# Performance work log

Hardware: AMD Instinct MI355X
Metric: run time of the kernel (lower is better)

Reference implementation:

```python
import jax, jax.numpy as jnp
import numpy as np

SIZE = 128      # reconstruction grid (size x size)
ANGLES = 128    # number of projection angles after interpolation
B, C, H, W = 2, 8, 128, 128  # batch, channels, detector rows (z-slices), detector cols
N_VIEWS = 8


def setup_inputs() -> dict:
    key = jax.random.key(0)
    keys = jax.random.split(key, N_VIEWS)
    return {f"f{i}": jax.random.normal(keys[i], (B, C, H, W), dtype=jnp.float32)
            for i in range(N_VIEWS)}


def _fbp(projections, size, n_angles):
    # projections: (B, C, H, V, W) -- V stacked views, W detector columns
    b, c, h, v, w = projections.shape
    # Interpolation step: resize V views -> n_angles angles (linear, half-pixel,
    # matching F.interpolate default semantics)
    sino = jax.image.resize(projections, (b, c, h, n_angles, w), method="linear")
    # Ram-Lak ramp filter along the detector-column axis
    ramp = jnp.abs(jnp.fft.fftfreq(w)).astype(jnp.float32)
    filt = jnp.real(jnp.fft.ifft(jnp.fft.fft(sino, axis=-1) * ramp, axis=-1)).astype(sino.dtype)
    # Back-projection (parallel beam, per z-slice H)
    thetas = jnp.arange(n_angles, dtype=jnp.float32) * (jnp.pi / n_angles)
    xs = jnp.arange(size, dtype=jnp.float32) - (size - 1) / 2.0
    X, Y = jnp.meshgrid(xs, xs, indexing="xy")  # (S, S)
    center = (w - 1) / 2.0

    sino_per_angle = jnp.moveaxis(filt, 3, 0)  # (A, B, C, H, W)

    def body(acc, inputs):
        theta, sino_a = inputs                       # sino_a: (B, C, H, W)
        t = X * jnp.cos(theta) + Y * jnp.sin(theta) + center  # (S, S)
        t = jnp.clip(t, 0.0, w - 1.0)
        t0 = jnp.floor(t).astype(jnp.int32)
        t1 = jnp.minimum(t0 + 1, w - 1)
        w1 = (t - t0).astype(sino_a.dtype)
        v0 = sino_a[..., t0]                         # (B, C, H, S, S) gather
        v1 = sino_a[..., t1]
        acc = acc + v0 * (1.0 - w1) + v1 * w1
        return acc, None

    acc0 = jnp.zeros((b, c, h, size, size), dtype=sino.dtype)
    vol, _ = jax.lax.scan(body, acc0, (thetas, sino_per_angle))
    return vol * (jnp.pi / (2.0 * n_angles))


def reference(f0, f1, f2, f3, f4, f5, f6, f7):
    # torch.cat([f.unsqueeze(3) for f in features], dim=3) == stack on new axis 3
    projections = jnp.stack([f0, f1, f2, f3, f4, f5, f6, f7], axis=3)  # (B,C,H,V,W)
    return _fbp(projections, SIZE, ANGLES)
```

## Files before the change

kernel.cpp:

```cpp
#include <hip/hip_runtime.h>
#include <math.h>

#define W 128
#define NANG 128
#define SZ 128
#define NV 8
#define NROWS 2048
#define K_DIM 1024
#define NPIX 16384
#define OUT_SCALE 0.012271846303085130f

typedef _Float16 f16x8 __attribute__((ext_vector_type(8)));
typedef _Float16 f16x4 __attribute__((ext_vector_type(4)));
typedef float    f32x4 __attribute__((ext_vector_type(4)));

#define PF_OFF 36864
#define WV_OFF (36864 + (size_t)NROWS * K_DIM * 2)

struct Ptrs8 { const float* p[8]; };

__device__ __forceinline__ void glds16(const void* g, void* l) {
    __builtin_amdgcn_global_load_lds(
        (const __attribute__((address_space(1))) void*)g,
        (__attribute__((address_space(3))) void*)l, 16, 0, 0);
}

#define FS_A 136
#define PREP_FG_BLOCKS 256

union PrepLds {
    struct {
        _Float16 sA[64 * FS_A];
        _Float16 sB[128 * FS_A];
        float    kl[W];
    } fg;
    struct {
        float  wrow[8 * K_DIM];
        float2 cst[NANG];
    } wv;
};

__global__ __launch_bounds__(256)
void k_prep(Ptrs8 in, _Float16* __restrict__ pf, _Float16* __restrict__ wv) {
    __shared__ PrepLds u;
    const int tid = threadIdx.x;

    if (blockIdx.x < PREP_FG_BLOCKS) {
        const int blk  = blockIdx.x;
        const int lane = tid & 63, wave = tid >> 6;
        const int fr = lane & 15, fg = lane >> 4;

        if (tid < W) {
            const int d = tid;
            const float w0 = 6.283185307179586f / (float)W * (float)d;
            float s = 0.f;
            for (int f = 1; f < 64; ++f)
                s = fmaf((float)f, __cosf(w0 * (float)f), s);
            s = 2.f * s + 64.f * ((d & 1) ? -1.f : 1.f);
            u.fg.kl[d] = s * (1.f / (float)(W * W));
        }
        {
            const int i   = tid >> 5;
            const int pos = (tid & 31) * 4;
#pragma unroll
            for (int v = 0; v < NV; ++v) {
                float4 x = *(const float4*)(in.p[v] + (size_t)(blk * 8 + i) * W + pos);
                f16x4 h = { (_Float16)x.x, (_Float16)x.y, (_Float16)x.z, (_Float16)x.w };
                *(f16x4*)&u.fg.sA[(i * 8 + v) * FS_A + pos] = h;
            }
        }
        __syncthreads();
        for (int e = tid; e < W * W; e += 256) {
            const int t = e >> 7, s = e & 127;
            u.fg.sB[t * FS_A + s] = (_Float16)u.fg.kl[(t - s) & (W - 1)];
        }
        __syncthreads();

        f32x4 acc[8] = {};
#pragma unroll
        for (int kb = 0; kb < W; kb += 32) {
            f16x8 af = *(const f16x8*)&u.fg.sA[(wave * 16 + fr) * FS_A + kb + fg * 8];
#pragma unroll
            for (int nt = 0; nt < 8; ++nt) {
                f16x8 bf = *(const f16x8*)&u.fg.sB[(nt * 16 + fr) * FS_A + kb + fg * 8];
                acc[nt] = __builtin_amdgcn_mfma_f32_16x16x32_f16(af, bf, acc[nt], 0, 0, 0);
            }
        }
#pragma unroll
        for (int nt = 0; nt < 8; ++nt) {
            int m = blk * 64 + wave * 16 + fg * 4;
            int n = nt * 16 + fr;
#pragma unroll
            for (int rr = 0; rr < 4; ++rr)
                pf[(size_t)(m + rr) * W + n] = (_Float16)acc[nt][rr];
        }
    } else {
        const int p0 = (blockIdx.x - PREP_FG_BLOCKS) * 8;
        if (tid < NANG) {
            float th = (float)tid * ((float)M_PI / (float)NANG);
            u.wv.cst[tid] = make_float2(cosf(th), sinf(th));
        }
        for (int i = tid; i < 8 * K_DIM; i += 256) u.wv.wrow[i] = 0.f;
        __syncthreads();
        const int px  = tid >> 5;
        const int sub = tid & 31;
        const int p = p0 + px;
        const float x = (float)(p & 127) - 63.5f;
        const float y = (float)(p >> 7) - 63.5f;
        float* prow = &u.wv.wrow[px * K_DIM];
        for (int a = sub; a < NANG; a += 32) {
            float2 c = u.wv.cst[a];
            float t = fmaf(x, c.x, fmaf(y, c.y, 63.5f));
            t = fminf(fmaxf(t, 0.f), 127.f);
            float tf = fminf(floorf(t), 126.f);
            int   ti = (int)tf;
            float wt = t - tf;
            float src = ((float)a + 0.5f) * 0.0625f - 0.5f;
            src = fminf(fmaxf(src, 0.f), 7.f);
            float vf = floorf(src);
            int   v0 = (int)vf;
            int   v1 = v0 + 1 < NV ? v0 + 1 : NV - 1;
            float wa = src - vf;
            float wA0 = (1.f - wa) * OUT_SCALE;
            atomicAdd(&prow[v0 * W + ti],     wA0 * (1.f - wt));
            atomicAdd(&prow[v0 * W + ti + 1], wA0 * wt);
            if (v1 != v0) {
                float wA1 = wa * OUT_SCALE;
                atomicAdd(&prow[v1 * W + ti],     wA1 * (1.f - wt));
                atomicAdd(&prow[v1 * W + ti + 1], wA1 * wt);
            }
        }
        __syncthreads();
        uint* wvu = (uint*)(wv + (size_t)p0 * K_DIM);
#pragma unroll
        for (int j = 0; j < 16; ++j) {
            int j2 = tid + 256 * j;
            float2 w2 = *(const float2*)&u.wv.wrow[j2 * 2];
            union { uint uu; struct { _Float16 lo, hi; } h; } pk;
            pk.h.lo = (_Float16)w2.x; pk.h.hi = (_Float16)w2.y;
            wvu[j2] = pk.uu;
        }
    }
}

#define NT 16

__device__ __forceinline__ void fencebar() {
    asm volatile("" ::: "memory");
    __builtin_amdgcn_s_barrier();
    asm volatile("" ::: "memory");
}

__device__ __forceinline__ void stage_half(const _Float16* __restrict__ G, int R0,
                                           int h, int kt, _Float16* L, int tid) {
#pragma unroll
    for (int r = 0; r < 2; ++r) {
        const int c   = r * 512 + tid;
        const int row = (h << 7) + (c >> 3);
        const int q   = c & 7;
        const _Float16* src = G + (size_t)(R0 + row) * K_DIM + kt * 64
                                + ((q ^ (row & 7)) << 3);
        _Float16* dst = L + (h << 13) + ((r * 512 + (tid & 448)) << 3);
        glds16(src, dst);
    }
}

__device__ __forceinline__ f16x8 frag(const _Float16* L, int row, int q) {
    return *(const f16x8*)(L + row * 64 + ((q ^ (row & 7)) << 3));
}

__global__ __launch_bounds__(512, 2)
void k_gemm(const _Float16* __restrict__ A,
            const _Float16* __restrict__ Bm,
            float* __restrict__ out) {
    __shared__ _Float16 lds[65536];
    const int tid  = threadIdx.x;
    const int lane = tid & 63, wid = tid >> 6;
    const int wm = wid >> 2, wn = wid & 3;
    const int fr = lane & 15, fg = lane >> 4;

    const int flat = blockIdx.y * 64 + blockIdx.x;
    const int x    = flat & 7;
    const int idx  = flat >> 3;
    const int m0 = (idx >> 3) * 256;
    const int n0 = (x * 8 + (idx & 7)) * 256;

    _Float16* const A0 = lds;
    _Float16* const B0 = lds + 16384;
    _Float16* const A1 = lds + 32768;
    _Float16* const B1 = lds + 49152;

    stage_half(Bm, n0, 0, 0, B0, tid);
    stage_half(A,  m0, 0, 0, A0, tid);
    stage_half(Bm, n0, 1, 0, B0, tid);
    stage_half(A,  m0, 1, 0, A0, tid);
    stage_half(Bm, n0, 0, 1, B1, tid);
    stage_half(A,  m0, 0, 1, A1, tid);
    asm volatile("s_waitcnt vmcnt(4)" ::: "memory");
    fencebar();

    f32x4 acc[8][4] = {};
    f16x8 af[4][2], bf[4][2];
    const int ar = wm * 128 + fr;
    const int br = wn * 64 + fr;

    auto tile = [&](int t, _Float16* Ab, _Float16* Bb, _Float16* An, _Float16* Bn)
        __attribute__((always_inline)) {
#pragma unroll
        for (int i = 0; i < 4; ++i) {
            af[i][0] = frag(Ab, ar + i * 16, fg);
            af[i][1] = frag(Ab, ar + i * 16, 4 + fg);
        }
#pragma unroll
        for (int j = 0; j < 2; ++j) {
            bf[j][0] = frag(Bb, br + j * 16, fg);
            bf[j][1] = frag(Bb, br + j * 16, 4 + fg);
        }
        if (t + 1 < NT) stage_half(Bm, n0, 1, t + 1, Bn, tid);
        fencebar();
        asm volatile("s_waitcnt lgkmcnt(0)" ::: "memory");
        __builtin_amdgcn_sched_barrier(0);
        __builtin_amdgcn_s_setprio(1);
#pragma unroll
        for (int i = 0; i < 4; ++i)
#pragma unroll
            for (int j = 0; j < 2; ++j) {
                acc[i][j] = __builtin_amdgcn_mfma_f32_16x16x32_f16(af[i][0], bf[j][0], acc[i][j], 0, 0, 0);
                acc[i][j] = __builtin_amdgcn_mfma_f32_16x16x32_f16(af[i][1], bf[j][1], acc[i][j], 0, 0, 0);
            }
        __builtin_amdgcn_s_setprio(0);
        fencebar();
#pragma unroll
        for (int j = 2; j < 4; ++j) {
            bf[j][0] = frag(Bb, br + j * 16, fg);
            bf[j][1] = frag(Bb, br + j * 16, 4 + fg);
        }
        if (t + 1 < NT) stage_half(A, m0, 1, t + 1, An, tid);
        fencebar();
        asm volatile("s_waitcnt lgkmcnt(0)" ::: "memory");
        __builtin_amdgcn_sched_barrier(0);
        __builtin_amdgcn_s_setprio(1);
#pragma unroll
        for (int i = 0; i < 4; ++i)
#pragma unroll
            for (int j = 2; j < 4; ++j) {
                acc[i][j] = __builtin_amdgcn_mfma_f32_16x16x32_f16(af[i][0], bf[j][0], acc[i][j], 0, 0, 0);
                acc[i][j] = __builtin_amdgcn_mfma_f32_16x16x32_f16(af[i][1], bf[j][1], acc[i][j], 0, 0, 0);
            }
        __builtin_amdgcn_s_setprio(0);
        fencebar();
#pragma unroll
        for (int i = 0; i < 4; ++i) {
            af[i][0] = frag(Ab, ar + 64 + i * 16, fg);
            af[i][1] = frag(Ab, ar + 64 + i * 16, 4 + fg);
        }
        if (t + 2 < NT) stage_half(Bm, n0, 0, t + 2, Bb, tid);
        fencebar();
        asm volatile("s_waitcnt lgkmcnt(0)" ::: "memory");
        __builtin_amdgcn_sched_barrier(0);
        __builtin_amdgcn_s_setprio(1);
#pragma unroll
        for (int i = 0; i < 4; ++i)
#pragma unroll
            for (int j = 2; j < 4; ++j) {
                acc[4 + i][j] = __builtin_amdgcn_mfma_f32_16x16x32_f16(af[i][0], bf[j][0], acc[4 + i][j], 0, 0, 0);
                acc[4 + i][j] = __builtin_amdgcn_mfma_f32_16x16x32_f16(af[i][1], bf[j][1], acc[4 + i][j], 0, 0, 0);
            }
        __builtin_amdgcn_s_setprio(0);
        fencebar();
        if (t + 2 < NT) stage_half(A, m0, 0, t + 2, Ab, tid);
        fencebar();
        __builtin_amdgcn_s_setprio(1);
#pragma unroll
        for (int i = 0; i < 4; ++i)
#pragma unroll
            for (int j = 0; j < 2; ++j) {
                acc[4 + i][j] = __builtin_amdgcn_mfma_f32_16x16x32_f16(af[i][0], bf[j][0], acc[4 + i][j], 0, 0, 0);
                acc[4 + i][j] = __builtin_amdgcn_mfma_f32_16x16x32_f16(af[i][1], bf[j][1], acc[4 + i][j], 0, 0, 0);
            }
        __builtin_amdgcn_s_setprio(0);
        if (t + 2 < NT)      asm volatile("s_waitcnt vmcnt(4)" ::: "memory");
        else if (t + 1 < NT) asm volatile("s_waitcnt vmcnt(0)" ::: "memory");
        fencebar();
    };

    for (int tt = 0; tt < NT; tt += 2) {
        tile(tt,     A0, B0, A1, B1);
        tile(tt + 1, A1, B1, A0, B0);
    }

#pragma unroll
    for (int i = 0; i < 8; ++i) {
#pragma unroll
        for (int j = 0; j < 4; ++j) {
            const int m = m0 + wm * 128 + i * 16 + fg * 4;
            const int n = n0 + wn * 64 + j * 16 + fr;
            float* op = out + (size_t)m * NPIX + n;
#pragma unroll
            for (int rr = 0; rr < 4; ++rr)
                op[(size_t)rr * NPIX] = acc[i][j][rr];
        }
    }
}

extern "C" void kernel_launch(void* const* d_in, const int* in_sizes, int n_in,
                              void* d_out, int out_size, void* d_ws, size_t ws_size,
                              hipStream_t stream) {
    _Float16*   pf = (_Float16*)((char*)d_ws + PF_OFF);
    _Float16*   wv = (_Float16*)((char*)d_ws + WV_OFF);

    Ptrs8 in;
    for (int i = 0; i < NV; ++i) in.p[i] = (const float*)d_in[i];

    k_prep<<<PREP_FG_BLOCKS + NPIX / 8, 256, 0, stream>>>(in, pf, wv);
    dim3 grid(NPIX / 256, NROWS / 256);
    k_gemm<<<grid, 512, 0, stream>>>(pf, wv, (float*)d_out);
}
```

Baseline: 261.6 us.

## Process two N tiles per block and overlap first tile's stores with second's compute

Each GEMM block now computes two adjacent 256-wide N tiles sequentially over a 32-step K pipeline, halving the grid to 256 blocks. The first tile's accumulators are copied to a second register set and written out in small chunks during the second tile's main loop, so output stores overlap MFMA work rather than forming a tail. The prefetch of the second tile's first K slices is chained into the pipeline without draining. This doubles accumulator register use, which may raise register pressure or cause spills, and halves the number of blocks available to fill the device.

```diff
diff --git a/kernel.cpp b/kernel.cpp
--- a/kernel.cpp
+++ b/kernel.cpp
@@ -143,7 +143,7 @@
     }
 }
 
-#define NT 16
+#define NT2 32
 
 __device__ __forceinline__ void fencebar() {
     asm volatile("" ::: "memory");
@@ -179,33 +179,38 @@
     const int wm = wid >> 2, wn = wid & 3;
     const int fr = lane & 15, fg = lane >> 4;
 
-    const int flat = blockIdx.y * 64 + blockIdx.x;
-    const int x    = flat & 7;
+    const int flat = blockIdx.x;
+    const int xcd  = flat & 7;
     const int idx  = flat >> 3;
-    const int m0 = (idx >> 3) * 256;
-    const int n0 = (x * 8 + (idx & 7)) * 256;
+    const int m0   = (idx & 7) * 256;
+    const int np   = xcd * 4 + (idx >> 3);
+    const int n0a  = np * 512;
+    const int n0b  = n0a + 256;
 
     _Float16* const A0 = lds;
     _Float16* const B0 = lds + 16384;
     _Float16* const A1 = lds + 32768;
     _Float16* const B1 = lds + 49152;
 
-    stage_half(Bm, n0, 0, 0, B0, tid);
-    stage_half(A,  m0, 0, 0, A0, tid);
-    stage_half(Bm, n0, 1, 0, B0, tid);
-    stage_half(A,  m0, 1, 0, A0, tid);
-    stage_half(Bm, n0, 0, 1, B1, tid);
-    stage_half(A,  m0, 0, 1, A1, tid);
+    stage_half(Bm, n0a, 0, 0, B0, tid);
+    stage_half(A,  m0,  0, 0, A0, tid);
+    stage_half(Bm, n0a, 1, 0, B0, tid);
+    stage_half(A,  m0,  1, 0, A0, tid);
+    stage_half(Bm, n0a, 0, 1, B1, tid);
+    stage_half(A,  m0,  0, 1, A1, tid);
     asm volatile("s_waitcnt vmcnt(4)" ::: "memory");
     fencebar();
 
     f32x4 acc[8][4] = {};
+    f32x4 sto[8][4] = {};
     f16x8 af[4][2], bf[4][2];
     const int ar = wm * 128 + fr;
     const int br = wn * 64 + fr;
 
-    auto tile = [&](int t, _Float16* Ab, _Float16* Bb, _Float16* An, _Float16* Bn)
-        __attribute__((always_inline)) {
+    auto tile = [&](int t, _Float16* Ab, _Float16* Bb, _Float16* An, _Float16* Bn,
+                    int nb1, int nb2, int c) __attribute__((always_inline)) {
+        const int s1 = (t + 1 < NT2), s2 = (t + 2 < NT2);
+        const int k1 = (t + 1) & 15, k2 = (t + 2) & 15;
 #pragma unroll
         for (int i = 0; i < 4; ++i) {
             af[i][0] = frag(Ab, ar + i * 16, fg);
@@ -216,7 +221,7 @@
             bf[j][0] = frag(Bb, br + j * 16, fg);
             bf[j][1] = frag(Bb, br + j * 16, 4 + fg);
         }
-        if (t + 1 < NT) stage_half(Bm, n0, 1, t + 1, Bn, tid);
+        if (s1) stage_half(Bm, nb1, 1, k1, Bn, tid);
         fencebar();
         asm volatile("s_waitcnt lgkmcnt(0)" ::: "memory");
         __builtin_amdgcn_sched_barrier(0);
@@ -235,7 +240,7 @@
             bf[j][0] = frag(Bb, br + j * 16, fg);
             bf[j][1] = frag(Bb, br + j * 16, 4 + fg);
         }
-        if (t + 1 < NT) stage_half(A, m0, 1, t + 1, An, tid);
+        if (s1) stage_half(A, m0, 1, k1, An, tid);
         fencebar();
         asm volatile("s_waitcnt lgkmcnt(0)" ::: "memory");
         __builtin_amdgcn_sched_barrier(0);
@@ -254,7 +259,7 @@
             af[i][0] = frag(Ab, ar + 64 + i * 16, fg);
             af[i][1] = frag(Ab, ar + 64 + i * 16, 4 + fg);
         }
-        if (t + 2 < NT) stage_half(Bm, n0, 0, t + 2, Bb, tid);
+        if (s2) stage_half(Bm, nb2, 0, k2, Bb, tid);
         fencebar();
         asm volatile("s_waitcnt lgkmcnt(0)" ::: "memory");
         __builtin_amdgcn_sched_barrier(0);
@@ -268,7 +273,7 @@
             }
         __builtin_amdgcn_s_setprio(0);
         fencebar();
-        if (t + 2 < NT) stage_half(A, m0, 0, t + 2, Ab, tid);
+        if (s2) stage_half(A, m0, 0, k2, Ab, tid);
         fencebar();
         __builtin_amdgcn_s_setprio(1);
 #pragma unroll
@@ -279,14 +284,61 @@
                 acc[4 + i][j] = __builtin_amdgcn_mfma_f32_16x16x32_f16(af[i][1], bf[j][1], acc[4 + i][j], 0, 0, 0);
             }
         __builtin_amdgcn_s_setprio(0);
-        if (t + 2 < NT)      asm volatile("s_waitcnt vmcnt(4)" ::: "memory");
-        else if (t + 1 < NT) asm volatile("s_waitcnt vmcnt(0)" ::: "memory");
+        if (c >= 0) {
+            const int mS = m0 + wm * 128;
+            const int nS = n0a + wn * 64;
+#define STORE_PP(pp)  {                                                        \
+            float* op = out + (size_t)(mS + ((pp) >> 2) * 16 + fg * 4) * NPIX  \
+                            + nS + ((pp) & 3) * 16 + fr;                       \
+            op[0]                = sto[(pp) >> 2][(pp) & 3][0];                \
+            op[(size_t)NPIX]     = sto[(pp) >> 2][(pp) & 3][1];                \
+            op[(size_t)2 * NPIX] = sto[(pp) >> 2][(pp) & 3][2];               \
+            op[(size_t)3 * NPIX] = sto[(pp) >> 2][(pp) & 3][3]; }
+            switch (c) {
+            case 0:  STORE_PP(0)  STORE_PP(1)  break;
+            case 1:  STORE_PP(2)  STORE_PP(3)  break;
+            case 2:  STORE_PP(4)  STORE_PP(5)  break;
+            case 3:  STORE_PP(6)  STORE_PP(7)  break;
+            case 4:  STORE_PP(8)  STORE_PP(9)  break;
+            case 5:  STORE_PP(10) STORE_PP(11) break;
+            case 6:  STORE_PP(12) STORE_PP(13) break;
+            case 7:  STORE_PP(14) STORE_PP(15) break;
+            case 8:  STORE_PP(16) STORE_PP(17) break;
+            case 9:  STORE_PP(18) STORE_PP(19) break;
+            case 10: STORE_PP(20) STORE_PP(21) break;
+            case 11: STORE_PP(22) STORE_PP(23) break;
+            case 12: STORE_PP(24) STORE_PP(25) break;
+            case 13: STORE_PP(26) STORE_PP(27) break;
+            case 14: STORE_PP(28) STORE_PP(29) break;
+            case 15: STORE_PP(30) STORE_PP(31) break;
+            }
+#undef STORE_PP
+        }
+        if (s2) {
+            if (c >= 0) asm volatile("s_waitcnt vmcnt(12)" ::: "memory");
+            else        asm volatile("s_waitcnt vmcnt(4)"  ::: "memory");
+        } else if (s1) {
+            if (c >= 0) asm volatile("s_waitcnt vmcnt(8)" ::: "memory");
+            else        asm volatile("s_waitcnt vmcnt(0)" ::: "memory");
+        }
         fencebar();
     };
 
-    for (int tt = 0; tt < NT; tt += 2) {
-        tile(tt,     A0, B0, A1, B1);
-        tile(tt + 1, A1, B1, A0, B0);
+    for (int tt = 0; tt < 16; tt += 2) {
+        const int u1 = tt + 1, u2 = tt + 2, u3 = tt + 3;
+        tile(tt,     A0, B0, A1, B1, (u1 < 16) ? n0a : n0b, (u2 < 16) ? n0a : n0b, -1);
+        tile(tt + 1, A1, B1, A0, B0, (u2 < 16) ? n0a : n0b, (u3 < 16) ? n0a : n0b, -1);
+    }
+#pragma unroll
+    for (int i = 0; i < 8; ++i)
+#pragma unroll
+        for (int j = 0; j < 4; ++j) {
+            sto[i][j] = acc[i][j];
+            acc[i][j] = (f32x4){0.f, 0.f, 0.f, 0.f};
+        }
+    for (int tt = 16; tt < 32; tt += 2) {
+        tile(tt,     A0, B0, A1, B1, n0b, n0b, tt - 16);
+        tile(tt + 1, A1, B1, A0, B0, n0b, n0b, tt - 15);
     }
 
 #pragma unroll
@@ -294,7 +346,7 @@
 #pragma unroll
         for (int j = 0; j < 4; ++j) {
             const int m = m0 + wm * 128 + i * 16 + fg * 4;
-            const int n = n0 + wn * 64 + j * 16 + fr;
+            const int n = n0b + wn * 64 + j * 16 + fr;
             float* op = out + (size_t)m * NPIX + n;
 #pragma unroll
             for (int rr = 0; rr < 4; ++rr)
@@ -313,6 +365,5 @@
     for (int i = 0; i < NV; ++i) in.p[i] = (const float*)d_in[i];
 
     k_prep<<<PREP_FG_BLOCKS + NPIX / 8, 256, 0, stream>>>(in, pf, wv);
-    dim3 grid(NPIX / 256, NROWS / 256);
-    k_gemm<<<grid, 512, 0, stream>>>(pf, wv, (float*)d_out);
-}
+    k_gemm<<<256, 512, 0, stream>>>(pf, wv, (float*)d_out);
+}
```

New measurement: 573.7 us. 119% more time.
